# Kernel tuning notes

Measured on AMD Instinct MI355X. Metric: run time of the kernel, lower is better.

The kernel has to match this reference:

```python
import jax, jax.numpy as jnp
import numpy as np

B, CIN, COUT, MODES, RES = 64, 64, 64, 16, 8192


def setup_inputs() -> dict:
    key = jax.random.key(0)
    kx, kr, ki = jax.random.split(key, 3)
    scale = 1.0 / (CIN * COUT)
    x = jax.random.normal(kx, (B, CIN, RES), dtype=jnp.float32)
    w_real = jax.random.normal(kr, (CIN, COUT, MODES), dtype=jnp.float32) * scale
    w_imag = jax.random.normal(ki, (CIN, COUT, MODES), dtype=jnp.float32) * scale
    return {"x": x, "w_real": w_real, "w_imag": w_imag}


def reference(x, w_real, w_imag):
    # x: [B, Cin, N] real; weight: [Cin, Cout, modes] complex
    batch, _, n = x.shape
    modes = w_real.shape[-1]
    cout = w_real.shape[1]
    w = w_real + 1j * w_imag
    x_ft = jnp.fft.rfft(x)                      # [B, Cin, N//2+1] complex64
    # single batched complex contraction over all kept modes
    out_modes = jnp.einsum('bim,iom->bom', x_ft[:, :, :modes], w)  # [B, Cout, modes]
    out_ft = jnp.zeros((batch, cout, x_ft.shape[-1]), dtype=out_modes.dtype)
    out_ft = out_ft.at[:, :, :modes].set(out_modes)
    return jnp.fft.irfft(out_ft, n=n)           # [B, Cout, N] real
```

## Files before the change

kernel.cpp:

```cpp
#include <hip/hip_runtime.h>
#include <math.h>


#define B_     64
#define CIN_   64
#define COUT_  64
#define MODES_ 16
#define RES_   8192
#define NA     512

__device__ static constexpr float COS16[16] = {
     1.0f,  0.92387953251128674f,  0.70710678118654752f,  0.38268343236508977f,
     0.0f, -0.38268343236508977f, -0.70710678118654752f, -0.92387953251128674f,
    -1.0f, -0.92387953251128674f, -0.70710678118654752f, -0.38268343236508977f,
     0.0f,  0.38268343236508977f,  0.70710678118654752f,  0.92387953251128674f
};
__device__ static constexpr float SIN16[16] = {
     0.0f,  0.38268343236508977f,  0.70710678118654752f,  0.92387953251128674f,
     1.0f,  0.92387953251128674f,  0.70710678118654752f,  0.38268343236508977f,
     0.0f, -0.38268343236508977f, -0.70710678118654752f, -0.92387953251128674f,
    -1.0f, -0.92387953251128674f, -0.70710678118654752f, -0.38268343236508977f
};

#define TWO_PI_OVER_RES 7.66990393942820428e-4f

__global__ __launch_bounds__(256) void kA(const float* __restrict__ x,
                                          float* __restrict__ X) {
    __shared__ float T[NA][20];
    __shared__ float P[16][16][2];
    const int row = blockIdx.x;
    const int tid = threadIdx.x;
    const float* __restrict__ xr = x + (size_t)row * RES_;

    for (int a = tid; a < NA; a += 256) {
        float xv[16];
#pragma unroll
        for (int b = 0; b < 16; ++b) xv[b] = xr[a + NA * b];
#pragma unroll
        for (int k = 0; k <= 8; ++k) {
            float sr = 0.f, si = 0.f;
#pragma unroll
            for (int b = 0; b < 16; ++b) {
                sr = fmaf(xv[b],  COS16[(k * b) & 15], sr);
                si = fmaf(xv[b], -SIN16[(k * b) & 15], si);
            }
            T[a][2 * k]     = sr;
            T[a][2 * k + 1] = si;
        }
    }
    __syncthreads();

    const int k = tid & 15;
    const int c = tid >> 4;
    const int kp = (k <= 8) ? k : 16 - k;
    const float sgn = (k <= 8) ? 1.f : -1.f;
    float accr = 0.f, acci = 0.f;
    for (int j = 0; j < 32; ++j) {
        const int a = c + 16 * j;
        const int m = (k * a) & (RES_ - 1);
        float sv, cv;
        __sincosf((float)m * TWO_PI_OVER_RES, &sv, &cv);
        const float tr = T[a][2 * kp];
        const float ti = sgn * T[a][2 * kp + 1];
        accr += cv * tr + sv * ti;
        acci += cv * ti - sv * tr;
    }
    P[k][c][0] = accr;
    P[k][c][1] = acci;
    __syncthreads();
    if (tid < 16) {
        float xre = 0.f, xim = 0.f;
#pragma unroll
        for (int c2 = 0; c2 < 16; ++c2) { xre += P[tid][c2][0]; xim += P[tid][c2][1]; }
        X[row * 32 + 2 * tid]     = xre;
        X[row * 32 + 2 * tid + 1] = xim;
    }
}

__global__ __launch_bounds__(256) void kB(const float* __restrict__ X,
                                          const float* __restrict__ wr,
                                          const float* __restrict__ wi,
                                          float* __restrict__ C) {
    __shared__ float Xs[CIN_][32];
    const int b = blockIdx.x;
    const int tid = threadIdx.x;
    const float* __restrict__ Xb = X + b * CIN_ * 32;
    for (int t = tid; t < CIN_ * 32; t += 256) ((float*)Xs)[t] = Xb[t];
    __syncthreads();

    const int k  = tid & 15;
    const int og = tid >> 4;
    float acc[4][2] = {};
    for (int i = 0; i < CIN_; ++i) {
        const float xre = Xs[i][2 * k];
        const float xim = Xs[i][2 * k + 1];
#pragma unroll
        for (int m = 0; m < 4; ++m) {
            const int o = og * 4 + m;
            const float wrv = wr[(i * COUT_ + o) * MODES_ + k];
            const float wiv = wi[(i * COUT_ + o) * MODES_ + k];
            acc[m][0] += xre * wrv - xim * wiv;
            acc[m][1] += xre * wiv + xim * wrv;
        }
    }
#pragma unroll
    for (int m = 0; m < 4; ++m) {
        const int o = og * 4 + m;
        C[((b * COUT_ + o) * MODES_ + k) * 2 + 0] = acc[m][0];
        C[((b * COUT_ + o) * MODES_ + k) * 2 + 1] = acc[m][1];
    }
}

__global__ __launch_bounds__(256) void kC(const float* __restrict__ C,
                                          float* __restrict__ y) {
    __shared__ float Cs[32];
    const int row = blockIdx.x;
    const int tid = threadIdx.x;
    if (tid < 32) Cs[tid] = C[row * 32 + tid];
    __syncthreads();
    float* __restrict__ yr = y + (size_t)row * RES_;

#pragma unroll
    for (int rep = 0; rep < 2; ++rep) {
        const int a = tid + rep * 256;
        float Dre[16], Dim[16];
#pragma unroll
        for (int k = 0; k < 16; ++k) {
            const int m = (k * a) & (RES_ - 1);
            float sv, cv;
            __sincosf((float)m * TWO_PI_OVER_RES, &sv, &cv);
            const float cr = Cs[2 * k], ci = Cs[2 * k + 1];
            const float g = (k == 0) ? (1.0f / RES_) : (2.0f / RES_);
            Dre[k] = g * (cr * cv - ci * sv);
            Dim[k] = g * (cr * sv + ci * cv);
        }
#pragma unroll
        for (int bb = 0; bb < 16; ++bb) {
            float v = 0.f;
#pragma unroll
            for (int k = 0; k < 16; ++k) {
                v = fmaf(Dre[k],  COS16[(k * bb) & 15], v);
                v = fmaf(Dim[k], -SIN16[(k * bb) & 15], v);
            }
            yr[a + NA * bb] = v;
        }
    }
}

extern "C" void kernel_launch(void* const* d_in, const int* in_sizes, int n_in,
                              void* d_out, int out_size, void* d_ws, size_t ws_size,
                              hipStream_t stream) {
    const float* x  = (const float*)d_in[0];
    const float* wr = (const float*)d_in[1];
    const float* wi = (const float*)d_in[2];
    float* out = (float*)d_out;

    float* X = (float*)d_ws;
    float* C = X + (size_t)B_ * CIN_ * 32;

    kA<<<dim3(B_ * CIN_), dim3(256), 0, stream>>>(x, X);
    kB<<<dim3(B_), dim3(256), 0, stream>>>(X, wr, wi, C);
    kC<<<dim3(B_ * COUT_), dim3(256), 0, stream>>>(C, out);
}
```

Before: 268.6 us.

## Fuse mode mixing into synthesis kernel, use twiddle recurrences and symmetric DFT16

Merges the channel-mixing kernel into the output synthesis kernel so each output row recomputes its 16 modes from the per-batch spectrum, removing one launch and the intermediate buffer. Both analysis and synthesis replace per-iteration sincos with complex rotation recurrences and exploit even/odd symmetry in the 16-point DFTs. Loads and stores are widened to float2/float4, and the shared-memory layout is transposed with padding to avoid bank conflicts. The recurrences can accumulate rounding error, and each synthesis block now redundantly reads the weights.

```diff
diff --git a/kernel.cpp b/kernel.cpp
--- a/kernel.cpp
+++ b/kernel.cpp
@@ -8,6 +8,7 @@
 #define MODES_ 16
 #define RES_   8192
 #define NA     512
+#define PITCH  522
 
 __device__ static constexpr float COS16[16] = {
      1.0f,  0.92387953251128674f,  0.70710678118654752f,  0.38268343236508977f,
@@ -22,48 +23,68 @@
     -1.0f, -0.92387953251128674f, -0.70710678118654752f, -0.38268343236508977f
 };
 
-#define TWO_PI_OVER_RES 7.66990393942820428e-4f
+#define W8192 7.66990393942820428e-4f
 
 __global__ __launch_bounds__(256) void kA(const float* __restrict__ x,
                                           float* __restrict__ X) {
-    __shared__ float T[NA][20];
-    __shared__ float P[16][16][2];
+    __shared__ float Ts[18 * PITCH];
+    __shared__ float P[16][17][2];
     const int row = blockIdx.x;
     const int tid = threadIdx.x;
     const float* __restrict__ xr = x + (size_t)row * RES_;
 
-    for (int a = tid; a < NA; a += 256) {
-        float xv[16];
-#pragma unroll
-        for (int b = 0; b < 16; ++b) xv[b] = xr[a + NA * b];
-#pragma unroll
-        for (int k = 0; k <= 8; ++k) {
-            float sr = 0.f, si = 0.f;
-#pragma unroll
-            for (int b = 0; b < 16; ++b) {
-                sr = fmaf(xv[b],  COS16[(k * b) & 15], sr);
-                si = fmaf(xv[b], -SIN16[(k * b) & 15], si);
-            }
-            T[a][2 * k]     = sr;
-            T[a][2 * k + 1] = si;
-        }
-    }
-    __syncthreads();
-
-    const int k = tid & 15;
-    const int c = tid >> 4;
+    float2 m[16];
+#pragma unroll
+    for (int b = 0; b < 16; ++b)
+        m[b] = *(const float2*)(xr + 2 * tid + NA * b);
+
+    float2 x0 = m[0], x8 = m[8];
+    float2 ev[8], ov[8];
+#pragma unroll
+    for (int b = 1; b <= 7; ++b) {
+        ev[b].x = m[b].x + m[16 - b].x;  ev[b].y = m[b].y + m[16 - b].y;
+        ov[b].x = m[b].x - m[16 - b].x;  ov[b].y = m[b].y - m[16 - b].y;
+    }
+#pragma unroll
+    for (int k = 0; k <= 8; ++k) {
+        float sr0 = (k & 1) ? (x0.x - x8.x) : (x0.x + x8.x);
+        float sr1 = (k & 1) ? (x0.y - x8.y) : (x0.y + x8.y);
+        float si0 = 0.f, si1 = 0.f;
+#pragma unroll
+        for (int b = 1; b <= 7; ++b) {
+            const float cc = COS16[(k * b) & 15];
+            const float ss = SIN16[(k * b) & 15];
+            sr0 = fmaf(ev[b].x, cc, sr0);
+            sr1 = fmaf(ev[b].y, cc, sr1);
+            si0 = fmaf(ov[b].x, -ss, si0);
+            si1 = fmaf(ov[b].y, -ss, si1);
+        }
+        *(float2*)&Ts[(2 * k) * PITCH + 2 * tid]     = make_float2(sr0, sr1);
+        *(float2*)&Ts[(2 * k + 1) * PITCH + 2 * tid] = make_float2(si0, si1);
+    }
+    __syncthreads();
+
+    const int k  = tid & 15;
+    const int c  = tid >> 4;
     const int kp = (k <= 8) ? k : 16 - k;
     const float sgn = (k <= 8) ? 1.f : -1.f;
+    float sA, cA, sB, cB;
+    __sincosf((float)(k * c)  * W8192, &sA, &cA);
+    __sincosf((float)(k * 16) * W8192, &sB, &cB);
+    float wre = cA, wim = -sA;
+    const float sre = cB, sim = -sB;
     float accr = 0.f, acci = 0.f;
+    const float* __restrict__ Tr = &Ts[(2 * kp) * PITCH + c];
+    const float* __restrict__ Ti = &Ts[(2 * kp + 1) * PITCH + c];
+#pragma unroll 8
     for (int j = 0; j < 32; ++j) {
-        const int a = c + 16 * j;
-        const int m = (k * a) & (RES_ - 1);
-        float sv, cv;
-        __sincosf((float)m * TWO_PI_OVER_RES, &sv, &cv);
-        const float tr = T[a][2 * kp];
-        const float ti = sgn * T[a][2 * kp + 1];
-        accr += cv * tr + sv * ti;
-        acci += cv * ti - sv * tr;
+        const float tr = Tr[16 * j];
+        const float ti = sgn * Ti[16 * j];
+        accr = fmaf(wre, tr, fmaf(-wim, ti, accr));
+        acci = fmaf(wre, ti, fmaf( wim, tr, acci));
+        const float nre = fmaf(wre, sre, -wim * sim);
+        wim = fmaf(wre, sim, wim * sre);
+        wre = nre;
     }
     P[k][c][0] = accr;
     P[k][c][1] = acci;
@@ -72,79 +93,101 @@
         float xre = 0.f, xim = 0.f;
 #pragma unroll
         for (int c2 = 0; c2 < 16; ++c2) { xre += P[tid][c2][0]; xim += P[tid][c2][1]; }
-        X[row * 32 + 2 * tid]     = xre;
-        X[row * 32 + 2 * tid + 1] = xim;
+        *(float2*)&X[row * 32 + 2 * tid] = make_float2(xre, xim);
     }
 }
 
-__global__ __launch_bounds__(256) void kB(const float* __restrict__ X,
+__global__ __launch_bounds__(256) void kC(const float* __restrict__ X,
                                           const float* __restrict__ wr,
                                           const float* __restrict__ wi,
-                                          float* __restrict__ C) {
-    __shared__ float Xs[CIN_][32];
-    const int b = blockIdx.x;
+                                          float* __restrict__ y) {
+    __shared__ float Xs[CIN_ * 32];
+    __shared__ float Ps[16][17][2];
+    __shared__ float Csh[32];
+    const int row = blockIdx.x;
+    const int b = row >> 6, o = row & 63;
     const int tid = threadIdx.x;
-    const float* __restrict__ Xb = X + b * CIN_ * 32;
-    for (int t = tid; t < CIN_ * 32; t += 256) ((float*)Xs)[t] = Xb[t];
-    __syncthreads();
-
-    const int k  = tid & 15;
-    const int og = tid >> 4;
-    float acc[4][2] = {};
-    for (int i = 0; i < CIN_; ++i) {
-        const float xre = Xs[i][2 * k];
-        const float xim = Xs[i][2 * k + 1];
-#pragma unroll
-        for (int m = 0; m < 4; ++m) {
-            const int o = og * 4 + m;
+
+    const float4* __restrict__ Xb4 = (const float4*)(X + (size_t)b * CIN_ * 32);
+    for (int t = tid; t < CIN_ * 8; t += 256)
+        ((float4*)Xs)[t] = Xb4[t];
+    __syncthreads();
+
+    {
+        const int k = tid & 15, p = tid >> 4;
+        float pr = 0.f, pi = 0.f;
+#pragma unroll
+        for (int mI = 0; mI < 4; ++mI) {
+            const int i = 4 * p + mI;
+            const float xre = Xs[i * 32 + 2 * k];
+            const float xim = Xs[i * 32 + 2 * k + 1];
             const float wrv = wr[(i * COUT_ + o) * MODES_ + k];
             const float wiv = wi[(i * COUT_ + o) * MODES_ + k];
-            acc[m][0] += xre * wrv - xim * wiv;
-            acc[m][1] += xre * wiv + xim * wrv;
-        }
-    }
-#pragma unroll
-    for (int m = 0; m < 4; ++m) {
-        const int o = og * 4 + m;
-        C[((b * COUT_ + o) * MODES_ + k) * 2 + 0] = acc[m][0];
-        C[((b * COUT_ + o) * MODES_ + k) * 2 + 1] = acc[m][1];
-    }
-}
-
-__global__ __launch_bounds__(256) void kC(const float* __restrict__ C,
-                                          float* __restrict__ y) {
-    __shared__ float Cs[32];
-    const int row = blockIdx.x;
-    const int tid = threadIdx.x;
-    if (tid < 32) Cs[tid] = C[row * 32 + tid];
-    __syncthreads();
+            pr = fmaf(xre, wrv, fmaf(-xim, wiv, pr));
+            pi = fmaf(xre, wiv, fmaf( xim, wrv, pi));
+        }
+        Ps[k][p][0] = pr;
+        Ps[k][p][1] = pi;
+    }
+    __syncthreads();
+    if (tid < 32) {
+        const int k = tid & 15, comp = tid >> 4;
+        float s = 0.f;
+#pragma unroll
+        for (int p = 0; p < 16; ++p) s += Ps[k][p][comp];
+        const float g = (k == 0) ? (1.0f / RES_) : (2.0f / RES_);
+        Csh[2 * k + comp] = g * s;
+    }
+    __syncthreads();
+
+    float C[32];
+#pragma unroll
+    for (int q = 0; q < 8; ++q) {
+        const float4 v = ((const float4*)Csh)[q];
+        C[4 * q] = v.x; C[4 * q + 1] = v.y; C[4 * q + 2] = v.z; C[4 * q + 3] = v.w;
+    }
+
     float* __restrict__ yr = y + (size_t)row * RES_;
-
-#pragma unroll
-    for (int rep = 0; rep < 2; ++rep) {
-        const int a = tid + rep * 256;
-        float Dre[16], Dim[16];
+    float yv[16][2];
+#pragma unroll
+    for (int half = 0; half < 2; ++half) {
+        const int a = 2 * tid + half;
+        float su, cu;
+        __sincosf((float)a * W8192, &su, &cu);
+        float wre = 1.f, wim = 0.f;
+        float Er0 = 0.f, Er8 = 0.f, Er[8], Oi[8];
+#pragma unroll
+        for (int q = 1; q <= 7; ++q) { Er[q] = 0.f; Oi[q] = 0.f; }
 #pragma unroll
         for (int k = 0; k < 16; ++k) {
-            const int m = (k * a) & (RES_ - 1);
-            float sv, cv;
-            __sincosf((float)m * TWO_PI_OVER_RES, &sv, &cv);
-            const float cr = Cs[2 * k], ci = Cs[2 * k + 1];
-            const float g = (k == 0) ? (1.0f / RES_) : (2.0f / RES_);
-            Dre[k] = g * (cr * cv - ci * sv);
-            Dim[k] = g * (cr * sv + ci * cv);
-        }
-#pragma unroll
-        for (int bb = 0; bb < 16; ++bb) {
-            float v = 0.f;
-#pragma unroll
-            for (int k = 0; k < 16; ++k) {
-                v = fmaf(Dre[k],  COS16[(k * bb) & 15], v);
-                v = fmaf(Dim[k], -SIN16[(k * bb) & 15], v);
+            const float cre = C[2 * k], cim = C[2 * k + 1];
+            const float dre = fmaf(cre, wre, -cim * wim);
+            const float dim = fmaf(cre, wim,  cim * wre);
+            if (k == 0)      { Er0 = dre; }
+            else if (k == 8) { Er8 = dre; }
+            else if (k < 8)  { Er[k]      += dre; Oi[k]      += dim; }
+            else             { Er[16 - k] += dre; Oi[16 - k] -= dim; }
+            const float nre = fmaf(wre, cu, -wim * su);
+            wim = fmaf(wre, su, wim * cu);
+            wre = nre;
+        }
+#pragma unroll
+        for (int bb = 0; bb <= 8; ++bb) {
+            float Cc = (bb & 1) ? (Er0 - Er8) : (Er0 + Er8);
+            float Ss = 0.f;
+#pragma unroll
+            for (int q = 1; q <= 7; ++q) {
+                Cc = fmaf(Er[q], COS16[(q * bb) & 15], Cc);
+                Ss = fmaf(Oi[q], SIN16[(q * bb) & 15], Ss);
             }
-            yr[a + NA * bb] = v;
-        }
-    }
+            if (bb == 0)      yv[0][half] = Cc;
+            else if (bb == 8) yv[8][half] = Cc;
+            else { yv[bb][half] = Cc - Ss; yv[16 - bb][half] = Cc + Ss; }
+        }
+    }
+#pragma unroll
+    for (int bb = 0; bb < 16; ++bb)
+        *(float2*)(yr + NA * bb + 2 * tid) = make_float2(yv[bb][0], yv[bb][1]);
 }
 
 extern "C" void kernel_launch(void* const* d_in, const int* in_sizes, int n_in,
@@ -154,11 +197,8 @@
     const float* wr = (const float*)d_in[1];
     const float* wi = (const float*)d_in[2];
     float* out = (float*)d_out;
-
     float* X = (float*)d_ws;
-    float* C = X + (size_t)B_ * CIN_ * 32;
 
     kA<<<dim3(B_ * CIN_), dim3(256), 0, stream>>>(x, X);
-    kB<<<dim3(B_), dim3(256), 0, stream>>>(X, wr, wi, C);
-    kC<<<dim3(B_ * COUT_), dim3(256), 0, stream>>>(C, out);
+    kC<<<dim3(B_ * COUT_), dim3(256), 0, stream>>>(X, wr, wi, out);
 }
```

After: 240.5 us. 1.12x faster.
